# Optimization experiments

Measured on AMD Instinct MI355X. Metric: run time of the kernel, lower is better.

The kernel has to match this reference:

```python
import jax, jax.numpy as jnp
import numpy as np

N_IN, D_IN, N_OUT, D_OUT = 1152, 8, 10, 16
ROUTINGS, NUM_BG = 3, 1
C, H, W = 1, 28, 28
BATCH = 128
DEC_IN = N_OUT * D_OUT  # 160, projection_type=None -> dec_feature_size = outcaps_size


def squash(x, axis=-1):
    norm = jnp.linalg.norm(x, axis=axis, keepdims=True)
    scale = norm ** 2 / (1.0 + norm ** 2) / (norm + 1e-8)
    return scale * x


def scale_coef(x, num_bg):
    # x: [B, n_out] or [B, n_out, n_in]; min/max normalize over dim 1,
    # excluding the last num_bg (background) capsules, then floor at 0.5.
    if num_bg > 0:
        xm = x[:, : x.shape[1] - num_bg]
    else:
        xm = x
    mn = jnp.min(xm, axis=1, keepdims=True)
    mx = jnp.max(xm, axis=1, keepdims=True)
    out = (xm - mn) / jnp.maximum(mx - mn, 1e-6)  # vrange (0,1)
    if num_bg > 0:
        out = jnp.concatenate([out, jnp.zeros_like(out[:, :num_bg])], axis=1)
    return jnp.maximum(out, 0.5)


def decode(capsflat, W1, b1, W2, b2, W3, b3):
    # fcn decoder (eval mode: dropout is identity): 160 -> 512 -> 1024 -> C*H*W
    h = jax.nn.relu(capsflat @ W1 + b1)
    h = jax.nn.relu(h @ W2 + b2)
    return jax.nn.sigmoid(h @ W3 + b3)


def setup_inputs() -> dict:
    key = jax.random.key(0)
    ks = jax.random.split(key, 9)
    return {
        'incaps': jax.random.normal(ks[0], (BATCH, N_IN, D_IN), jnp.float32),
        'x_input': jax.random.uniform(ks[1], (BATCH, C, H, W), jnp.float32),
        'weight': 0.1 * jax.random.normal(ks[2], (N_OUT, N_IN, D_OUT, D_IN), jnp.float32),
        'W1': 0.05 * jax.random.normal(ks[3], (DEC_IN, 512), jnp.float32),
        'b1': jnp.zeros((512,), jnp.float32),
        'W2': 0.05 * jax.random.normal(ks[4], (512, 1024), jnp.float32),
        'b2': jnp.zeros((1024,), jnp.float32),
        'W3': 0.05 * jax.random.normal(ks[5], (1024, C * H * W), jnp.float32),
        'b3': jnp.zeros((C * H * W,), jnp.float32),
    }


def reference(incaps, x_input, weight, W1, b1, W2, b2, W3, b3):
    B = incaps.shape[0]
    # outcaps_hat: matmul(weight, incaps[:,None,:,:,None]).squeeze(-1)
    hat = jnp.einsum('nkoi,bki->bnko', weight, incaps)  # [B, n_out, n_in, d_out]
    hat_d = jax.lax.stop_gradient(hat)
    rc = jnp.ones((B, N_OUT, N_IN), hat.dtype)
    eye = jnp.eye(N_OUT, dtype=hat.dtype)
    x_flat = x_input.reshape(B, 1, -1)
    for _ in range(ROUTINGS - 1):
        # squash over capsule dim, weighted sum over input capsules
        outcaps = squash(jnp.sum(rc[..., None] * hat_d, axis=2, keepdims=True))  # [B,n,1,d]
        b = jnp.sum(outcaps * hat_d, axis=-1)  # agreement [B, n_out, n_in]
        c = scale_coef(b, NUM_BG)
        objcaps = outcaps[:, :, 0, :]  # [B, n_out, d_out]
        # get_every_obj_rscore vectorized: mask one object capsule at a time
        masked = objcaps[:, None, :, :] * eye[None, :, :, None]  # [B, n_obj, n_out, d]
        recon = decode(masked.reshape(B, N_OUT, DEC_IN), W1, b1, W2, b2, W3, b3)  # [B,n_obj,CHW]
        rscore = -jnp.sum((x_flat - recon) ** 2, axis=-1)  # neg MSE-sum, [B, n_obj]
        r = scale_coef(rscore, NUM_BG)
        rc = c * r[:, :, None]
    # final iteration uses non-detached hat
    outcaps = squash(jnp.sum(rc[..., None] * hat, axis=2, keepdims=True))
    return outcaps[:, :, 0, :]  # [B, n_out, d_out]
```

## Files before the change

kernel.cpp:

```cpp
#include <hip/hip_runtime.h>
#include <math.h>

#define BATCH  128
#define NIN    1152
#define DIN    8
#define NOUTC  10
#define DOUT   16
#define H1DIM  512
#define H2DIM  1024
#define PIX    784
#define NROWS  (BATCH * NOUTC)
#define NBY3   13

typedef __attribute__((ext_vector_type(8))) __bf16 bf16x8;
typedef __attribute__((ext_vector_type(4))) float  f32x4;
typedef __attribute__((ext_vector_type(4))) unsigned int u32x4;

__device__ __forceinline__ float bf2f(unsigned int u) {
    union { unsigned int i; float f; } v; v.i = u << 16; return v.f;
}
__device__ __forceinline__ ushort f2bf(float f) {
    union { float f; unsigned int i; } v; v.f = f;
    unsigned int r = v.i + 0x7FFFu + ((v.i >> 16) & 1u);
    return (ushort)(r >> 16);
}
__device__ __forceinline__ float ldin(const void* p, size_t i, int isbf) {
    return isbf ? bf2f(((const ushort*)p)[i]) : ((const float*)p)[i];
}
__device__ __forceinline__ bf16x8 frag_of(uint4 u) {
    return __builtin_bit_cast(bf16x8, u);
}
__device__ __forceinline__ bf16x8 ld_frag(const ushort* p) {
    return frag_of(*(const uint4*)p);
}
__device__ __forceinline__ float dot8(uint4 a, uint4 b) {
    float s;
    s  = bf2f(a.x & 0xffffu) * bf2f(b.x & 0xffffu);
    s += bf2f(a.x >> 16)     * bf2f(b.x >> 16);
    s += bf2f(a.y & 0xffffu) * bf2f(b.y & 0xffffu);
    s += bf2f(a.y >> 16)     * bf2f(b.y >> 16);
    s += bf2f(a.z & 0xffffu) * bf2f(b.z & 0xffffu);
    s += bf2f(a.z >> 16)     * bf2f(b.z >> 16);
    s += bf2f(a.w & 0xffffu) * bf2f(b.w & 0xffffu);
    s += bf2f(a.w >> 16)     * bf2f(b.w >> 16);
    return s;
}
__device__ __forceinline__ uint4 pack8(float4 a, float4 b) {
    uint4 r;
    r.x = f2bf(a.x) | ((unsigned)f2bf(a.y) << 16);
    r.y = f2bf(a.z) | ((unsigned)f2bf(a.w) << 16);
    r.z = f2bf(b.x) | ((unsigned)f2bf(b.y) << 16);
    r.w = f2bf(b.z) | ((unsigned)f2bf(b.w) << 16);
    return r;
}

__device__ __forceinline__ int detect_bf(const void* w, int* cntS) {
    int tid = threadIdx.x, nt = blockDim.x;
    if (tid == 0) *cntS = 0;
    __syncthreads();
    const ushort* u = (const ushort*)w;
    int c = 0;
    for (int s = tid; s < 512; s += nt) {
        int e = (u[s * 2] >> 7) & 0xFF;
        if (e >= 88 && e <= 140) c++;
    }
    atomicAdd(cntS, c);
    __syncthreads();
    return (*cntS >= 384) ? 1 : 0;
}

struct PrepArgs {
    const void* w;
    const void* src[7];
    ushort*     dst[7];
    int         n[7];
    int*        flag;
};

__global__ __launch_bounds__(256) void prep_kernel(PrepArgs a)
{
    __shared__ int cntS;
    __shared__ ushort tile[32][33];
    int tid = threadIdx.x;
    int isbf = detect_bf(a.w, &cntS);
    int seg = blockIdx.y;
    if (seg == 0 && blockIdx.x == 0 && tid == 0) *a.flag = isbf;

    if (seg <= 4) {
        int n = a.n[seg];
        int stride = gridDim.x * 256;
        ushort* d = a.dst[seg];
        if (isbf) {
            const ushort* s = (const ushort*)a.src[seg];
            for (int i = blockIdx.x * 256 + tid; i < n; i += stride) d[i] = s[i];
        } else {
            const float* s = (const float*)a.src[seg];
            for (int i = blockIdx.x * 256 + tid; i < n; i += stride) d[i] = f2bf(s[i]);
        }
        return;
    }
    int R = (seg == 5) ? H1DIM : H2DIM;
    int C = (seg == 5) ? H2DIM : PIX;
    int tilesX = (seg == 5) ? 32 : 25;
    int tilesY = (seg == 5) ? 16 : 32;
    int t = blockIdx.x;
    if (t >= tilesX * tilesY) return;
    int tx2 = t % tilesX, ty2 = t / tilesX;
    int c0 = tx2 * 32, r0 = ty2 * 32;
    const void* in = a.src[seg];
    ushort* out = a.dst[seg];
    int tx = tid & 31, ty = tid >> 5;
    for (int i = ty; i < 32; i += 8) {
        int r = r0 + i, c = c0 + tx;
        tile[i][tx] = (r < R && c < C) ? f2bf(ldin(in, (size_t)r * C + c, isbf)) : (ushort)0;
    }
    __syncthreads();
    for (int i = ty; i < 32; i += 8) {
        int c = c0 + i, r = r0 + tx;
        if (c < C && r < R) out[(size_t)c * R + r] = tile[tx][i];
    }
}

__global__ __launch_bounds__(256) void hat_build(
    const void* __restrict__ inc,
    const void* __restrict__ w,
    ushort* __restrict__ hatG)
{
    __shared__ int cntS;
    int isbf = detect_bf(w, &cntS);
    int kc = blockIdx.x, bc = blockIdx.y, n = blockIdx.z;
    int t  = threadIdx.x;
    int k  = kc * 128 + (t >> 1);
    int oh = (t & 1) << 3;

    size_t wbase = ((size_t)n * NIN + k) * DOUT + oh;
    uint4 wr[8];
    if (isbf) {
        const uint4* wp = (const uint4*)((const ushort*)w + wbase * DIN);
        #pragma unroll
        for (int j = 0; j < 8; j++) wr[j] = wp[j];
    } else {
        const float4* wp = (const float4*)((const float*)w + wbase * DIN);
        #pragma unroll
        for (int j = 0; j < 8; j++) wr[j] = pack8(wp[2 * j], wp[2 * j + 1]);
    }

    int b0 = bc * 16;
    #pragma unroll 4
    for (int bl = 0; bl < 16; bl++) {
        int b = b0 + bl;
        size_t ioff = ((size_t)b * NIN + k) * DIN;
        uint4 iu;
        if (isbf) iu = *(const uint4*)((const ushort*)inc + ioff);
        else {
            const float4* ip = (const float4*)((const float*)inc + ioff);
            iu = pack8(ip[0], ip[1]);
        }
        unsigned int h[8];
        #pragma unroll
        for (int j = 0; j < 8; j++) h[j] = f2bf(dot8(wr[j], iu));
        u32x4 ov = { h[0] | (h[1] << 16), h[2] | (h[3] << 16),
                     h[4] | (h[5] << 16), h[6] | (h[7] << 16) };
        __builtin_nontemporal_store(ov,
            (u32x4*)(hatG + (((size_t)(b * NOUTC + n) * NIN + k) * DOUT + oh)));
    }
}

template<bool COMPUTE>
__global__ __launch_bounds__(512, 4) void reduce_pass(
    const ushort* __restrict__ hatG,
    const void*   __restrict__ incRaw,
    const void*   __restrict__ wRaw,
    const ushort* __restrict__ bsPrev,
    const float*  __restrict__ partials,
    int iter0,
    const ushort* __restrict__ W1c,
    const ushort* __restrict__ b1c,
    ushort* __restrict__ h1out,
    ushort* __restrict__ bsOut,
    void*   __restrict__ outFinal,
    const int* __restrict__ flagp)
{
    int bn  = blockIdx.x;
    int n   = bn % NOUTC;
    int b   = bn / NOUTC;
    int tid = threadIdx.x;

    __shared__ ushort wSb[NIN];
    __shared__ float  redS[8][16];
    __shared__ float  sumS[16];
    __shared__ float  ocS[16];
    __shared__ float  scaleS;

    int h = tid & 1, kb = tid >> 1;
    int wave = tid >> 6, lane = tid & 63;

    uint4 v[4];
    const ushort* tailS;

    if constexpr (!COMPUTE) {
        __shared__ uint4 hatTail4[256];
        const ushort* hbase = hatG + (size_t)bn * NIN * DOUT;
        #pragma unroll
        for (int j = 0; j < 4; j++)
            v[j] = *(const uint4*)(hbase + ((kb + 256 * j) * DOUT + h * 8));
        if (tid < 256)
            hatTail4[tid] = *(const uint4*)(hbase + 1024 * DOUT + tid * 8);
        tailS = (const ushort*)hatTail4;
    } else {
        __shared__ int cntS;
        __shared__ uint4 hatS4[NIN * DOUT / 8];
        int isbf = detect_bf(wRaw, &cntS);
        size_t wnb = (size_t)n * NIN * DOUT * DIN;
        for (int idx = tid; idx < NIN * DOUT; idx += 512) {
            int k = idx >> 4;
            float s = 0.f;
            #pragma unroll
            for (int i = 0; i < 8; i++)
                s += ldin(wRaw, wnb + (size_t)idx * 8 + i, isbf) *
                     ldin(incRaw, ((size_t)b * NIN + k) * DIN + i, isbf);
            ((ushort*)hatS4)[idx] = f2bf(s);
        }
        __syncthreads();
        const ushort* hbase = (const ushort*)hatS4;
        #pragma unroll
        for (int j = 0; j < 4; j++)
            v[j] = *(const uint4*)(hbase + ((kb + 256 * j) * DOUT + h * 8));
        tailS = hbase + 1024 * DOUT;
    }

    if (!iter0) {
        if (tid < 9) {
            float s = 0.f;
            #pragma unroll
            for (int j = 0; j < NBY3; j++)
                s += partials[(size_t)(b * NOUTC + tid) * 16 + j];
            sumS[tid] = -s;
        }
        __syncthreads();
        float mn = 1e30f, mx = -1e30f;
        #pragma unroll
        for (int n2 = 0; n2 < 9; n2++) {
            float vv = sumS[n2];
            mn = fminf(mn, vv); mx = fmaxf(mx, vv);
        }
        float den = fmaxf(mx - mn, 1e-6f);
        float rv = (n < 9) ? fmaxf((sumS[n] - mn) / den, 0.5f) : 0.5f;
        for (int k = tid; k < NIN; k += 512) {
            float c = 0.5f;
            if (n < 9) {
                float vv[9], mn2 = 1e30f, mx2 = -1e30f;
                #pragma unroll
                for (int n2 = 0; n2 < 9; n2++) {
                    vv[n2] = bf2f(bsPrev[(size_t)(b * NOUTC + n2) * NIN + k]);
                    mn2 = fminf(mn2, vv[n2]); mx2 = fmaxf(mx2, vv[n2]);
                }
                float den2 = fmaxf(mx2 - mn2, 1e-6f);
                c = fmaxf((vv[n] - mn2) / den2, 0.5f);
            }
            wSb[k] = f2bf(c * rv);
        }
    }
    __syncthreads();

    float acc[8];
    #pragma unroll
    for (int o = 0; o < 8; o++) acc[o] = 0.f;
    #pragma unroll
    for (int j = 0; j < 4; j++) {
        int k = kb + 256 * j;
        float w = iter0 ? 1.f : bf2f(wSb[k]);
        bf16x8 hv = frag_of(v[j]);
        #pragma unroll
        for (int o = 0; o < 8; o++) acc[o] += w * (float)hv[o];
    }
    if (tid < 256) {
        int k = 1024 + kb;
        float w = iter0 ? 1.f : bf2f(wSb[k]);
        bf16x8 hv = ld_frag(tailS + kb * DOUT + h * 8);
        #pragma unroll
        for (int o = 0; o < 8; o++) acc[o] += w * (float)hv[o];
    }
    #pragma unroll
    for (int off = 32; off >= 2; off >>= 1) {
        #pragma unroll
        for (int o = 0; o < 8; o++) acc[o] += __shfl_xor(acc[o], off);
    }
    if (lane < 2) {
        #pragma unroll
        for (int o = 0; o < 8; o++) redS[wave][lane * 8 + o] = acc[o];
    }
    __syncthreads();
    if (tid < 16) {
        float s = 0.f;
        #pragma unroll
        for (int wv = 0; wv < 8; wv++) s += redS[wv][tid];
        sumS[tid] = s;
    }
    __syncthreads();
    if (tid == 0) {
        float n2 = 0.f;
        #pragma unroll
        for (int o = 0; o < 16; o++) n2 += sumS[o] * sumS[o];
        float nrm = sqrtf(n2);
        scaleS = n2 / (1.f + n2) / (nrm + 1e-8f);
    }
    __syncthreads();
    if (tid < 16) {
        float oc = scaleS * sumS[tid];
        ocS[tid] = oc;
        if (outFinal) {
            if (*flagp) ((ushort*)outFinal)[(size_t)bn * 16 + tid] = f2bf(oc);
            else        ((float*) outFinal)[(size_t)bn * 16 + tid] = oc;
        }
    }
    __syncthreads();

    if (bsOut) {
        float o0 = ocS[h * 8 + 0], o1 = ocS[h * 8 + 1], o2 = ocS[h * 8 + 2],
              o3 = ocS[h * 8 + 3], o4 = ocS[h * 8 + 4], o5 = ocS[h * 8 + 5],
              o6 = ocS[h * 8 + 6], o7 = ocS[h * 8 + 7];
        #pragma unroll
        for (int j = 0; j < 4; j++) {
            bf16x8 hv = frag_of(v[j]);
            float s = o0 * (float)hv[0] + o1 * (float)hv[1] + o2 * (float)hv[2] +
                      o3 * (float)hv[3] + o4 * (float)hv[4] + o5 * (float)hv[5] +
                      o6 * (float)hv[6] + o7 * (float)hv[7];
            s += __shfl_xor(s, 1);
            if (h == 0) bsOut[(size_t)bn * NIN + kb + 256 * j] = f2bf(s);
        }
        if (tid < 256) {
            bf16x8 hv = ld_frag(tailS + kb * DOUT + h * 8);
            float s = o0 * (float)hv[0] + o1 * (float)hv[1] + o2 * (float)hv[2] +
                      o3 * (float)hv[3] + o4 * (float)hv[4] + o5 * (float)hv[5] +
                      o6 * (float)hv[6] + o7 * (float)hv[7];
            s += __shfl_xor(s, 1);
            if (h == 0) bsOut[(size_t)bn * NIN + 1024 + kb] = f2bf(s);
        }
    }

    if (h1out) {
        int col = tid;
        float acc1 = bf2f(b1c[col]);
        #pragma unroll
        for (int i = 0; i < 16; i++)
            acc1 += ocS[i] * bf2f(W1c[(size_t)(n * 16 + i) * H1DIM + col]);
        h1out[(size_t)bn * H1DIM + col] = f2bf(fmaxf(acc1, 0.f));
    }
}

__global__ __launch_bounds__(256) void gemm_kernel(
    const ushort* __restrict__ A, const ushort* __restrict__ Bt,
    const ushort* __restrict__ bias, int K, int N,
    ushort* __restrict__ Cout,
    const ushort* __restrict__ xin, float* __restrict__ partials)
{
    int m0 = blockIdx.x * 64, n0 = blockIdx.y * 64;
    int tid = threadIdx.x;
    int wave = tid >> 6, lane = tid & 63, quad = lane >> 4, l16 = lane & 15;

    __shared__ uint4 As4[320];
    __shared__ uint4 Bs4[320];
    ushort* As = (ushort*)As4;
    ushort* Bs = (ushort*)Bs4;

    f32x4 acc[4];
    #pragma unroll
    for (int nt = 0; nt < 4; nt++)
        #pragma unroll
        for (int rg = 0; rg < 4; rg++) acc[nt][rg] = 0.f;

    int sMi = tid >> 2, sKk = (tid & 3) * 8;
    int sLds = sMi * 5 + (tid & 3);
    const ushort* Ap = A + (size_t)(m0 + sMi) * K + sKk;
    const ushort* Bp = Bt + (size_t)(n0 + sMi) * K + sKk;
    bool bOK = (n0 + sMi) < N;

    uint4 aR = *(const uint4*)Ap;
    uint4 bR = bOK ? *(const uint4*)Bp : make_uint4(0, 0, 0, 0);

    for (int k0 = 0; k0 < K; k0 += 32) {
        As4[sLds] = aR;
        Bs4[sLds] = bR;
        __syncthreads();
        if (k0 + 32 < K) {
            aR = *(const uint4*)(Ap + k0 + 32);
            bR = bOK ? *(const uint4*)(Bp + k0 + 32) : make_uint4(0, 0, 0, 0);
        }
        bf16x8 a = ld_frag(As + (wave * 16 + l16) * 40 + quad * 8);
        #pragma unroll
        for (int nt = 0; nt < 4; nt++) {
            bf16x8 bb = ld_frag(Bs + (nt * 16 + l16) * 40 + quad * 8);
            acc[nt] = __builtin_amdgcn_mfma_f32_16x16x32_bf16(a, bb, acc[nt], 0, 0, 0);
        }
        __syncthreads();
    }

    int rowBase = m0 + wave * 16 + quad * 4;
    if (Cout) {
        #pragma unroll
        for (int nt = 0; nt < 4; nt++) {
            int col = n0 + nt * 16 + l16;
            float bv = bf2f(bias[col]);
            #pragma unroll
            for (int rg = 0; rg < 4; rg++) {
                float v = acc[nt][rg] + bv;
                Cout[(size_t)(rowBase + rg) * N + col] = f2bf(fmaxf(v, 0.f));
            }
        }
    } else {
        float vr[4] = {0.f, 0.f, 0.f, 0.f};
        #pragma unroll
        for (int nt = 0; nt < 4; nt++) {
            int col = n0 + nt * 16 + l16;
            if (col < N) {
                float bv = bf2f(bias[col]);
                #pragma unroll
                for (int rg = 0; rg < 4; rg++) {
                    int row = rowBase + rg;
                    int bb = row / NOUTC;
                    float z = acc[nt][rg] + bv;
                    float s = 1.f / (1.f + __expf(-z));
                    float d = bf2f(xin[(size_t)bb * PIX + col]) - s;
                    vr[rg] += d * d;
                }
            }
        }
        #pragma unroll
        for (int rg = 0; rg < 4; rg++) {
            float v = vr[rg];
            #pragma unroll
            for (int off = 8; off >= 1; off >>= 1) v += __shfl_xor(v, off, 16);
            if (l16 == 0)
                partials[(size_t)(rowBase + rg) * 16 + blockIdx.y] = v;
        }
    }
}

extern "C" void kernel_launch(void* const* d_in, const int* in_sizes, int n_in,
                              void* d_out, int out_size, void* d_ws, size_t ws_size,
                              hipStream_t stream)
{
    const void* inc = d_in[0];
    const void* x   = d_in[1];
    const void* w   = d_in[2];
    const void* W1  = d_in[3];
    const void* b1  = d_in[4];
    const void* W2  = d_in[5];
    const void* b2  = d_in[6];
    const void* W3  = d_in[7];
    const void* b3  = d_in[8];

    char* p = (char*)d_ws;
    auto alloc = [&](size_t bytes) { void* r = p; p += (bytes + 255) & ~(size_t)255; return r; };
    int*    flagWS    = (int*)alloc(256);
    ushort* bsA       = (ushort*)alloc((size_t)NROWS * NIN * 2);
    ushort* bsB       = (ushort*)alloc((size_t)NROWS * NIN * 2);
    float*  partials  = (float*)alloc((size_t)NROWS * 16 * 4);
    ushort* h1WS      = (ushort*)alloc((size_t)NROWS * H1DIM * 2);
    ushort* h2WS      = (ushort*)alloc((size_t)NROWS * H2DIM * 2);
    ushort* W2T       = (ushort*)alloc((size_t)H2DIM * H1DIM * 2);
    ushort* W3T       = (ushort*)alloc((size_t)PIX * H2DIM * 2);
    ushort* W1c       = (ushort*)alloc((size_t)160 * H1DIM * 2);
    ushort* b1c       = (ushort*)alloc((size_t)H1DIM * 2);
    ushort* b2c       = (ushort*)alloc((size_t)H2DIM * 2);
    ushort* b3c       = (ushort*)alloc((size_t)PIX * 2);
    ushort* xc        = (ushort*)alloc((size_t)BATCH * PIX * 2);
    ushort* hatG      = (ushort*)alloc((size_t)NROWS * NIN * DOUT * 2);
    bool haveHat = ((char*)hatG + (size_t)NROWS * NIN * DOUT * 2) <= ((char*)d_ws + ws_size);

    PrepArgs pa;
    pa.w = w;
    pa.src[0] = W1;  pa.dst[0] = W1c;  pa.n[0] = 160 * H1DIM;
    pa.src[1] = b1;  pa.dst[1] = b1c;  pa.n[1] = H1DIM;
    pa.src[2] = b2;  pa.dst[2] = b2c;  pa.n[2] = H2DIM;
    pa.src[3] = b3;  pa.dst[3] = b3c;  pa.n[3] = PIX;
    pa.src[4] = x;   pa.dst[4] = xc;   pa.n[4] = BATCH * PIX;
    pa.src[5] = W2;  pa.dst[5] = W2T;  pa.n[5] = 0;
    pa.src[6] = W3;  pa.dst[6] = W3T;  pa.n[6] = 0;
    pa.flag = flagWS;
    prep_kernel<<<dim3(800, 7), 256, 0, stream>>>(pa);

    if (haveHat) hat_build<<<dim3(9, 8, NOUTC), 256, 0, stream>>>(inc, w, hatG);

    if (haveHat)
        reduce_pass<false><<<NROWS, 512, 0, stream>>>(
            hatG, inc, w, nullptr, nullptr, 1,
            W1c, b1c, h1WS, bsA, nullptr, flagWS);
    else
        reduce_pass<true><<<NROWS, 512, 0, stream>>>(
            nullptr, inc, w, nullptr, nullptr, 1,
            W1c, b1c, h1WS, bsA, nullptr, flagWS);

    for (int it = 0; it < 2; it++) {
        gemm_kernel<<<dim3(NROWS / 64, H2DIM / 64), 256, 0, stream>>>(
            h1WS, W2T, b2c, H1DIM, H2DIM, h2WS, nullptr, nullptr);
        gemm_kernel<<<dim3(NROWS / 64, NBY3), 256, 0, stream>>>(
            h2WS, W3T, b3c, H2DIM, PIX, nullptr, xc, partials);

        int last = (it == 1);
        const ushort* bsP = (it == 0) ? bsA : bsB;
        ushort* bsO       = last ? nullptr : bsB;
        ushort* h1o       = last ? nullptr : h1WS;
        void*   fin       = last ? d_out : nullptr;
        if (haveHat)
            reduce_pass<false><<<NROWS, 512, 0, stream>>>(
                hatG, inc, w, bsP, partials, 0,
                W1c, b1c, h1o, bsO, fin, flagWS);
        else
            reduce_pass<true><<<NROWS, 512, 0, stream>>>(
                nullptr, inc, w, bsP, partials, 0,
                W1c, b1c, h1o, bsO, fin, flagWS);
    }
}
```

Before: 213.2 us.

## Skip background-capsule decoder rows, precompute routing coefficients, merge hat build into prep

The decoder GEMMs now run on only the 9 object capsules per batch (BATCH*9 rows instead of BATCH*10), since the background capsule's reconstruction score is never used. The per-input-capsule min/max normalization of agreements moves out of reduce_pass into extra blocks of the layer-2 GEMM launch, which write a coefficient buffer so the reduce only does one load and multiply per element. The hat-building kernel is folded into prep_kernel as an extra segment, saving one launch and one format-detection pass. Together these reduce decoder FLOPs and repeated 9-way loads in the reduce, at the cost of another buffer and heavier non-uniform work inside the GEMM and prep grids.

New measurement: 217.7 us. 2.1% more time.

```diff
diff --git a/kernel.cpp b/kernel.cpp
--- a/kernel.cpp
+++ b/kernel.cpp
@@ -10,6 +10,7 @@
 #define H2DIM  1024
 #define PIX    784
 #define NROWS  (BATCH * NOUTC)
+#define MROWS  (BATCH * 9)
 #define NBY3   13
 
 typedef __attribute__((ext_vector_type(8))) __bf16 bf16x8;
@@ -53,7 +54,6 @@
     r.w = f2bf(b.z) | ((unsigned)f2bf(b.w) << 16);
     return r;
 }
-
 __device__ __forceinline__ int detect_bf(const void* w, int* cntS) {
     int tid = threadIdx.x, nt = blockDim.x;
     if (tid == 0) *cntS = 0;
@@ -71,6 +71,8 @@
 
 struct PrepArgs {
     const void* w;
+    const void* inc;
+    ushort*     hatG;
     const void* src[7];
     ushort*     dst[7];
     int         n[7];
@@ -96,6 +98,44 @@
         } else {
             const float* s = (const float*)a.src[seg];
             for (int i = blockIdx.x * 256 + tid; i < n; i += stride) d[i] = f2bf(s[i]);
+        }
+        return;
+    }
+    if (seg == 7) {
+        if (!a.hatG || blockIdx.x >= 720) return;
+        int u = blockIdx.x;
+        int kc = u % 9, r = u / 9, bc = r % 8, n = r / 8;
+        int k = kc * 128 + (tid >> 1);
+        int oh = (tid & 1) << 3;
+        size_t wbase = ((size_t)n * NIN + k) * DOUT + oh;
+        uint4 wr[8];
+        if (isbf) {
+            const uint4* wp = (const uint4*)((const ushort*)a.w + wbase * DIN);
+            #pragma unroll
+            for (int j = 0; j < 8; j++) wr[j] = wp[j];
+        } else {
+            const float4* wp = (const float4*)((const float*)a.w + wbase * DIN);
+            #pragma unroll
+            for (int j = 0; j < 8; j++) wr[j] = pack8(wp[2 * j], wp[2 * j + 1]);
+        }
+        int b0 = bc * 16;
+        #pragma unroll 4
+        for (int bl = 0; bl < 16; bl++) {
+            int b = b0 + bl;
+            size_t ioff = ((size_t)b * NIN + k) * DIN;
+            uint4 iu;
+            if (isbf) iu = *(const uint4*)((const ushort*)a.inc + ioff);
+            else {
+                const float4* ip = (const float4*)((const float*)a.inc + ioff);
+                iu = pack8(ip[0], ip[1]);
+            }
+            unsigned int h[8];
+            #pragma unroll
+            for (int j = 0; j < 8; j++) h[j] = f2bf(dot8(wr[j], iu));
+            u32x4 ov = { h[0] | (h[1] << 16), h[2] | (h[3] << 16),
+                         h[4] | (h[5] << 16), h[6] | (h[7] << 16) };
+            __builtin_nontemporal_store(ov,
+                (u32x4*)(a.hatG + (((size_t)(b * NOUTC + n) * NIN + k) * DOUT + oh)));
         }
         return;
     }
@@ -121,57 +161,12 @@
     }
 }
 
-__global__ __launch_bounds__(256) void hat_build(
-    const void* __restrict__ inc,
-    const void* __restrict__ w,
-    ushort* __restrict__ hatG)
-{
-    __shared__ int cntS;
-    int isbf = detect_bf(w, &cntS);
-    int kc = blockIdx.x, bc = blockIdx.y, n = blockIdx.z;
-    int t  = threadIdx.x;
-    int k  = kc * 128 + (t >> 1);
-    int oh = (t & 1) << 3;
-
-    size_t wbase = ((size_t)n * NIN + k) * DOUT + oh;
-    uint4 wr[8];
-    if (isbf) {
-        const uint4* wp = (const uint4*)((const ushort*)w + wbase * DIN);
-        #pragma unroll
-        for (int j = 0; j < 8; j++) wr[j] = wp[j];
-    } else {
-        const float4* wp = (const float4*)((const float*)w + wbase * DIN);
-        #pragma unroll
-        for (int j = 0; j < 8; j++) wr[j] = pack8(wp[2 * j], wp[2 * j + 1]);
-    }
-
-    int b0 = bc * 16;
-    #pragma unroll 4
-    for (int bl = 0; bl < 16; bl++) {
-        int b = b0 + bl;
-        size_t ioff = ((size_t)b * NIN + k) * DIN;
-        uint4 iu;
-        if (isbf) iu = *(const uint4*)((const ushort*)inc + ioff);
-        else {
-            const float4* ip = (const float4*)((const float*)inc + ioff);
-            iu = pack8(ip[0], ip[1]);
-        }
-        unsigned int h[8];
-        #pragma unroll
-        for (int j = 0; j < 8; j++) h[j] = f2bf(dot8(wr[j], iu));
-        u32x4 ov = { h[0] | (h[1] << 16), h[2] | (h[3] << 16),
-                     h[4] | (h[5] << 16), h[6] | (h[7] << 16) };
-        __builtin_nontemporal_store(ov,
-            (u32x4*)(hatG + (((size_t)(b * NOUTC + n) * NIN + k) * DOUT + oh)));
-    }
-}
-
 template<bool COMPUTE>
 __global__ __launch_bounds__(512, 4) void reduce_pass(
     const ushort* __restrict__ hatG,
     const void*   __restrict__ incRaw,
     const void*   __restrict__ wRaw,
-    const ushort* __restrict__ bsPrev,
+    const ushort* __restrict__ cbuf,
     const float*  __restrict__ partials,
     int iter0,
     const ushort* __restrict__ W1c,
@@ -234,7 +229,7 @@
             float s = 0.f;
             #pragma unroll
             for (int j = 0; j < NBY3; j++)
-                s += partials[(size_t)(b * NOUTC + tid) * 16 + j];
+                s += partials[(size_t)(b * 9 + tid) * 16 + j];
             sumS[tid] = -s;
         }
         __syncthreads();
@@ -246,20 +241,9 @@
         }
         float den = fmaxf(mx - mn, 1e-6f);
         float rv = (n < 9) ? fmaxf((sumS[n] - mn) / den, 0.5f) : 0.5f;
-        for (int k = tid; k < NIN; k += 512) {
-            float c = 0.5f;
-            if (n < 9) {
-                float vv[9], mn2 = 1e30f, mx2 = -1e30f;
-                #pragma unroll
-                for (int n2 = 0; n2 < 9; n2++) {
-                    vv[n2] = bf2f(bsPrev[(size_t)(b * NOUTC + n2) * NIN + k]);
-                    mn2 = fminf(mn2, vv[n2]); mx2 = fmaxf(mx2, vv[n2]);
-                }
-                float den2 = fmaxf(mx2 - mn2, 1e-6f);
-                c = fmaxf((vv[n] - mn2) / den2, 0.5f);
-            }
-            wSb[k] = f2bf(c * rv);
-        }
+        const ushort* crow = cbuf + (size_t)bn * NIN;
+        for (int k = tid; k < NIN; k += 512)
+            wSb[k] = f2bf(bf2f(crow[k]) * rv);
     }
     __syncthreads();
 
@@ -316,7 +300,7 @@
     }
     __syncthreads();
 
-    if (bsOut) {
+    if (bsOut && n < 9) {
         float o0 = ocS[h * 8 + 0], o1 = ocS[h * 8 + 1], o2 = ocS[h * 8 + 2],
               o3 = ocS[h * 8 + 3], o4 = ocS[h * 8 + 4], o5 = ocS[h * 8 + 5],
               o6 = ocS[h * 8 + 6], o7 = ocS[h * 8 + 7];
@@ -339,20 +323,100 @@
         }
     }
 
-    if (h1out) {
+    if (h1out && n < 9) {
         int col = tid;
         float acc1 = bf2f(b1c[col]);
         #pragma unroll
         for (int i = 0; i < 16; i++)
             acc1 += ocS[i] * bf2f(W1c[(size_t)(n * 16 + i) * H1DIM + col]);
-        h1out[(size_t)bn * H1DIM + col] = f2bf(fmaxf(acc1, 0.f));
-    }
-}
-
-__global__ __launch_bounds__(256) void gemm_kernel(
+        h1out[(size_t)(b * 9 + n) * H1DIM + col] = f2bf(fmaxf(acc1, 0.f));
+    }
+}
+
+__global__ __launch_bounds__(256) void gemm2_kernel(
     const ushort* __restrict__ A, const ushort* __restrict__ Bt,
-    const ushort* __restrict__ bias, int K, int N,
-    ushort* __restrict__ Cout,
+    const ushort* __restrict__ bias, ushort* __restrict__ Cout,
+    const ushort* __restrict__ bs, ushort* __restrict__ cbuf)
+{
+    if (blockIdx.y >= 16) {
+        int ci = (blockIdx.y - 16) * 18 + blockIdx.x;
+        int base = ci * 4096 + threadIdx.x;
+        #pragma unroll 4
+        for (int j = 0; j < 16; j++) {
+            int pi = base + j * 256;
+            int b = pi / NIN, k = pi - b * NIN;
+            const ushort* bp = bs + (size_t)b * NOUTC * NIN + k;
+            float vv[9], mn = 1e30f, mx = -1e30f;
+            #pragma unroll
+            for (int n2 = 0; n2 < 9; n2++) {
+                vv[n2] = bf2f(bp[n2 * NIN]);
+                mn = fminf(mn, vv[n2]); mx = fmaxf(mx, vv[n2]);
+            }
+            float den = fmaxf(mx - mn, 1e-6f);
+            ushort* cp = cbuf + (size_t)b * NOUTC * NIN + k;
+            #pragma unroll
+            for (int n2 = 0; n2 < 9; n2++)
+                cp[n2 * NIN] = f2bf(fmaxf((vv[n2] - mn) / den, 0.5f));
+            cp[9 * NIN] = f2bf(0.5f);
+        }
+        return;
+    }
+    int m0 = blockIdx.x * 64, n0 = blockIdx.y * 64;
+    int tid = threadIdx.x;
+    int wave = tid >> 6, lane = tid & 63, quad = lane >> 4, l16 = lane & 15;
+
+    __shared__ uint4 As4[320];
+    __shared__ uint4 Bs4[320];
+    ushort* As = (ushort*)As4;
+    ushort* Bs = (ushort*)Bs4;
+
+    f32x4 acc[4];
+    #pragma unroll
+    for (int nt = 0; nt < 4; nt++)
+        #pragma unroll
+        for (int rg = 0; rg < 4; rg++) acc[nt][rg] = 0.f;
+
+    int sMi = tid >> 2, sKk = (tid & 3) * 8;
+    int sLds = sMi * 5 + (tid & 3);
+    const ushort* Ap = A + (size_t)(m0 + sMi) * H1DIM + sKk;
+    const ushort* Bp = Bt + (size_t)(n0 + sMi) * H1DIM + sKk;
+
+    uint4 aR = *(const uint4*)Ap;
+    uint4 bR = *(const uint4*)Bp;
+
+    for (int k0 = 0; k0 < H1DIM; k0 += 32) {
+        As4[sLds] = aR;
+        Bs4[sLds] = bR;
+        __syncthreads();
+        if (k0 + 32 < H1DIM) {
+            aR = *(const uint4*)(Ap + k0 + 32);
+            bR = *(const uint4*)(Bp + k0 + 32);
+        }
+        bf16x8 a = ld_frag(As + (wave * 16 + l16) * 40 + quad * 8);
+        #pragma unroll
+        for (int nt = 0; nt < 4; nt++) {
+            bf16x8 bb = ld_frag(Bs + (nt * 16 + l16) * 40 + quad * 8);
+            acc[nt] = __builtin_amdgcn_mfma_f32_16x16x32_bf16(a, bb, acc[nt], 0, 0, 0);
+        }
+        __syncthreads();
+    }
+
+    int rowBase = m0 + wave * 16 + quad * 4;
+    #pragma unroll
+    for (int nt = 0; nt < 4; nt++) {
+        int col = n0 + nt * 16 + l16;
+        float bv = bf2f(bias[col]);
+        #pragma unroll
+        for (int rg = 0; rg < 4; rg++) {
+            float v = acc[nt][rg] + bv;
+            Cout[(size_t)(rowBase + rg) * H2DIM + col] = f2bf(fmaxf(v, 0.f));
+        }
+    }
+}
+
+__global__ __launch_bounds__(256) void gemm3_kernel(
+    const ushort* __restrict__ A, const ushort* __restrict__ Bt,
+    const ushort* __restrict__ bias,
     const ushort* __restrict__ xin, float* __restrict__ partials)
 {
     int m0 = blockIdx.x * 64, n0 = blockIdx.y * 64;
@@ -372,18 +436,18 @@
 
     int sMi = tid >> 2, sKk = (tid & 3) * 8;
     int sLds = sMi * 5 + (tid & 3);
-    const ushort* Ap = A + (size_t)(m0 + sMi) * K + sKk;
-    const ushort* Bp = Bt + (size_t)(n0 + sMi) * K + sKk;
-    bool bOK = (n0 + sMi) < N;
+    const ushort* Ap = A + (size_t)(m0 + sMi) * H2DIM + sKk;
+    const ushort* Bp = Bt + (size_t)(n0 + sMi) * H2DIM + sKk;
+    bool bOK = (n0 + sMi) < PIX;
 
     uint4 aR = *(const uint4*)Ap;
     uint4 bR = bOK ? *(const uint4*)Bp : make_uint4(0, 0, 0, 0);
 
-    for (int k0 = 0; k0 < K; k0 += 32) {
+    for (int k0 = 0; k0 < H2DIM; k0 += 32) {
         As4[sLds] = aR;
         Bs4[sLds] = bR;
         __syncthreads();
-        if (k0 + 32 < K) {
+        if (k0 + 32 < H2DIM) {
             aR = *(const uint4*)(Ap + k0 + 32);
             bR = bOK ? *(const uint4*)(Bp + k0 + 32) : make_uint4(0, 0, 0, 0);
         }
@@ -397,43 +461,30 @@
     }
 
     int rowBase = m0 + wave * 16 + quad * 4;
-    if (Cout) {
-        #pragma unroll
-        for (int nt = 0; nt < 4; nt++) {
-            int col = n0 + nt * 16 + l16;
+    float vr[4] = {0.f, 0.f, 0.f, 0.f};
+    #pragma unroll
+    for (int nt = 0; nt < 4; nt++) {
+        int col = n0 + nt * 16 + l16;
+        if (col < PIX) {
             float bv = bf2f(bias[col]);
             #pragma unroll
             for (int rg = 0; rg < 4; rg++) {
-                float v = acc[nt][rg] + bv;
-                Cout[(size_t)(rowBase + rg) * N + col] = f2bf(fmaxf(v, 0.f));
+                int row = rowBase + rg;
+                int bb = row / 9;
+                float z = acc[nt][rg] + bv;
+                float s = 1.f / (1.f + __expf(-z));
+                float d = bf2f(xin[(size_t)bb * PIX + col]) - s;
+                vr[rg] += d * d;
             }
         }
-    } else {
-        float vr[4] = {0.f, 0.f, 0.f, 0.f};
-        #pragma unroll
-        for (int nt = 0; nt < 4; nt++) {
-            int col = n0 + nt * 16 + l16;
-            if (col < N) {
-                float bv = bf2f(bias[col]);
-                #pragma unroll
-                for (int rg = 0; rg < 4; rg++) {
-                    int row = rowBase + rg;
-                    int bb = row / NOUTC;
-                    float z = acc[nt][rg] + bv;
-                    float s = 1.f / (1.f + __expf(-z));
-                    float d = bf2f(xin[(size_t)bb * PIX + col]) - s;
-                    vr[rg] += d * d;
-                }
-            }
-        }
-        #pragma unroll
-        for (int rg = 0; rg < 4; rg++) {
-            float v = vr[rg];
-            #pragma unroll
-            for (int off = 8; off >= 1; off >>= 1) v += __shfl_xor(v, off, 16);
-            if (l16 == 0)
-                partials[(size_t)(rowBase + rg) * 16 + blockIdx.y] = v;
-        }
+    }
+    #pragma unroll
+    for (int rg = 0; rg < 4; rg++) {
+        float v = vr[rg];
+        #pragma unroll
+        for (int off = 8; off >= 1; off >>= 1) v += __shfl_xor(v, off, 16);
+        if (l16 == 0)
+            partials[(size_t)(rowBase + rg) * 16 + blockIdx.y] = v;
     }
 }
 
@@ -454,11 +505,11 @@
     char* p = (char*)d_ws;
     auto alloc = [&](size_t bytes) { void* r = p; p += (bytes + 255) & ~(size_t)255; return r; };
     int*    flagWS    = (int*)alloc(256);
-    ushort* bsA       = (ushort*)alloc((size_t)NROWS * NIN * 2);
-    ushort* bsB       = (ushort*)alloc((size_t)NROWS * NIN * 2);
-    float*  partials  = (float*)alloc((size_t)NROWS * 16 * 4);
-    ushort* h1WS      = (ushort*)alloc((size_t)NROWS * H1DIM * 2);
-    ushort* h2WS      = (ushort*)alloc((size_t)NROWS * H2DIM * 2);
+    ushort* bs        = (ushort*)alloc((size_t)NROWS * NIN * 2);
+    ushort* cbuf      = (ushort*)alloc((size_t)NROWS * NIN * 2);
+    float*  partials  = (float*)alloc((size_t)MROWS * 16 * 4);
+    ushort* h1WS      = (ushort*)alloc((size_t)MROWS * H1DIM * 2);
+    ushort* h2WS      = (ushort*)alloc((size_t)MROWS * H2DIM * 2);
     ushort* W2T       = (ushort*)alloc((size_t)H2DIM * H1DIM * 2);
     ushort* W3T       = (ushort*)alloc((size_t)PIX * H2DIM * 2);
     ushort* W1c       = (ushort*)alloc((size_t)160 * H1DIM * 2);
@@ -470,7 +521,7 @@
     bool haveHat = ((char*)hatG + (size_t)NROWS * NIN * DOUT * 2) <= ((char*)d_ws + ws_size);
 
     PrepArgs pa;
-    pa.w = w;
+    pa.w = w; pa.inc = inc; pa.hatG = haveHat ? hatG : nullptr;
     pa.src[0] = W1;  pa.dst[0] = W1c;  pa.n[0] = 160 * H1DIM;
     pa.src[1] = b1;  pa.dst[1] = b1c;  pa.n[1] = H1DIM;
     pa.src[2] = b2;  pa.dst[2] = b2c;  pa.n[2] = H2DIM;
@@ -479,37 +530,34 @@
     pa.src[5] = W2;  pa.dst[5] = W2T;  pa.n[5] = 0;
     pa.src[6] = W3;  pa.dst[6] = W3T;  pa.n[6] = 0;
     pa.flag = flagWS;
-    prep_kernel<<<dim3(800, 7), 256, 0, stream>>>(pa);
-
-    if (haveHat) hat_build<<<dim3(9, 8, NOUTC), 256, 0, stream>>>(inc, w, hatG);
+    prep_kernel<<<dim3(800, 8), 256, 0, stream>>>(pa);
 
     if (haveHat)
         reduce_pass<false><<<NROWS, 512, 0, stream>>>(
             hatG, inc, w, nullptr, nullptr, 1,
-            W1c, b1c, h1WS, bsA, nullptr, flagWS);
+            W1c, b1c, h1WS, bs, nullptr, flagWS);
     else
         reduce_pass<true><<<NROWS, 512, 0, stream>>>(
             nullptr, inc, w, nullptr, nullptr, 1,
-            W1c, b1c, h1WS, bsA, nullptr, flagWS);
+            W1c, b1c, h1WS, bs, nullptr, flagWS);
 
     for (int it = 0; it < 2; it++) {
-        gemm_kernel<<<dim3(NROWS / 64, H2DIM / 64), 256, 0, stream>>>(
-            h1WS, W2T, b2c, H1DIM, H2DIM, h2WS, nullptr, nullptr);
-        gemm_kernel<<<dim3(NROWS / 64, NBY3), 256, 0, stream>>>(
-            h2WS, W3T, b3c, H2DIM, PIX, nullptr, xc, partials);
+        gemm2_kernel<<<dim3(18, 18), 256, 0, stream>>>(
+            h1WS, W2T, b2c, h2WS, bs, cbuf);
+        gemm3_kernel<<<dim3(18, NBY3), 256, 0, stream>>>(
+            h2WS, W3T, b3c, xc, partials);
 
         int last = (it == 1);
-        const ushort* bsP = (it == 0) ? bsA : bsB;
-        ushort* bsO       = last ? nullptr : bsB;
-        ushort* h1o       = last ? nullptr : h1WS;
-        void*   fin       = last ? d_out : nullptr;
+        ushort* bsO = last ? nullptr : bs;
+        ushort* h1o = last ? nullptr : h1WS;
+        void*   fin = last ? d_out : nullptr;
         if (haveHat)
             reduce_pass<false><<<NROWS, 512, 0, stream>>>(
-                hatG, inc, w, bsP, partials, 0,
+                hatG, inc, w, cbuf, partials, 0,
                 W1c, b1c, h1o, bsO, fin, flagWS);
         else
             reduce_pass<true><<<NROWS, 512, 0, stream>>>(
-                nullptr, inc, w, bsP, partials, 0,
+                nullptr, inc, w, cbuf, partials, 0,
                 W1c, b1c, h1o, bsO, fin, flagWS);
     }
 }
```
